# Optimization experiments

Measured on AMD Instinct MI355X. Metric: run time of the kernel, lower is better.

Reference implementation:

```python
import jax, jax.numpy as jnp
import numpy as np

MAX_RADIUS = 10.0
NUM_BASIS = 3
H = 100
C = 32  # dim(Rs_hidden) with scalar-only irreps
LEAKY_SLOPE = 0.01

def swish(v):
    return v * jax.nn.sigmoid(v)


def setup_inputs() -> dict:
    key = jax.random.key(0)
    ks = jax.random.split(key, 10)
    B, N = 4, 256
    x = jax.random.normal(ks[0], (B, N, C), dtype=jnp.float32)
    xyz = jax.random.normal(ks[1], (B, N, 3), dtype=jnp.float32) * 3.0
    mask = jax.random.randint(ks[2], (B, N), 0, 2).astype(jnp.int64)
    # radial MLP (GaussianRadialModel): basis(3) -> h(100) -> C*C path weights
    rw1 = jax.random.normal(ks[3], (NUM_BASIS, H), dtype=jnp.float32) / np.sqrt(NUM_BASIS)
    rw2 = jax.random.normal(ks[4], (H, C * C), dtype=jnp.float32) / np.sqrt(H)
    # fc3: Linear(C, C); fc2: Linear(C, 1)
    fc3_w = jax.random.normal(ks[5], (C, C), dtype=jnp.float32) / np.sqrt(C)
    fc3_b = jax.random.normal(ks[6], (C,), dtype=jnp.float32) * 0.01
    fc2_w = jax.random.normal(ks[7], (C, 1), dtype=jnp.float32) / np.sqrt(C)
    fc2_b = jax.random.normal(ks[8], (1,), dtype=jnp.float32) * 0.01
    return {"x": x, "xyz": xyz, "mask": mask, "rw1": rw1, "rw2": rw2,
            "fc3_w": fc3_w, "fc3_b": fc3_b, "fc2_w": fc2_w, "fc2_b": fc2_b}


def _normalize(v, eps=1e-6):
    mean = jnp.mean(v, axis=-1, keepdims=True)
    std = jnp.std(v, axis=-1, keepdims=True, ddof=1)  # torch std is unbiased
    return (v - mean) / (std + eps)


def reference(x, xyz, mask, rw1, rw2, fc3_w, fc3_b, fc2_w, fc2_b):
    B, N, Cc = x.shape
    # --- fc1: e3nn point convolution with Gaussian radial kernel (l=0 paths) ---
    diff = xyz[:, :, None, :] - xyz[:, None, :, :]            # [B,N,N,3]
    r = jnp.sqrt(jnp.sum(diff * diff, axis=-1) + 1e-12)       # [B,N,N]
    spacing = MAX_RADIUS / NUM_BASIS
    centers = jnp.linspace(0.0, MAX_RADIUS, NUM_BASIS, dtype=jnp.float32)
    gamma = 1.0 / spacing
    basis = jnp.exp(-gamma * (r[..., None] - centers) ** 2)   # [B,N,N,3]
    hid = swish(jnp.einsum('zabk,kh->zabh', basis, rw1))      # [B,N,N,H]
    K = jnp.einsum('zabh,hf->zabf', hid, rw2).reshape(B, N, N, Cc, Cc)  # per-pair kernel
    out = jnp.einsum('zabij,zbj->zai', K, x) / jnp.sqrt(jnp.float32(N))  # [B,N,C]
    # --- Norm(Rs_hidden): per-irrep L2 norm; for l=0 channels this is |x| ---
    out = jnp.abs(out)
    # --- mask + sum pool over points ---
    out = jnp.where(mask[..., None] == 0, 0.0, out)
    pooled = jnp.sum(out, axis=1)                             # [B,C]
    pooled = _normalize(pooled)
    # --- MLP head: leaky_relu(fc3) -> fc2 -> flatten ---
    h1 = pooled @ fc3_w + fc3_b
    h1 = jnp.where(h1 >= 0, h1, LEAKY_SLOPE * h1)
    y = h1 @ fc2_w + fc2_b                                    # [B,1]
    return y.reshape(-1)
```

## Files before the change

### kernel.cpp

```cpp
#include <hip/hip_runtime.h>
#include <math.h>

#define GAMMA 0.3f
#define WSTR3 424

typedef __bf16 bf16x8 __attribute__((ext_vector_type(8)));
typedef __bf16 bf16x4 __attribute__((ext_vector_type(4)));
typedef float  f32x4  __attribute__((ext_vector_type(4)));

__global__ __launch_bounds__(256, 4) void k2_fused(const float* __restrict__ x,
                                                   const float* __restrict__ xyz,
                                                   const float* __restrict__ rw1,
                                                   const float* __restrict__ rw2,
                                                   float* __restrict__ part) {
    __shared__ __bf16 Wlds[32 * WSTR3];
    __shared__ float  rw1s[304];

    int bid = blockIdx.x;
    int ah = bid & 3;
    int hh = (bid >> 2) & 3;
    int bc = (bid >> 4) & 15;
    int z  = bid >> 8;
    int t  = threadIdx.x;
    int w  = t >> 6;
    int l  = t & 63;
    int l16 = l & 15, lg = l >> 4;

    for (int e = t; e < 300; e += 256) rw1s[e] = rw1[e];
    if (t < 128) {
        int icol = t >> 2, g = t & 3;
        *(bf16x4*)&Wlds[icol * WSTR3 + 12 * 32 + g * 8 + 4] = (bf16x4){(__bf16)0.f, (__bf16)0.f, (__bf16)0.f, (__bf16)0.f};
    }

    int a_glob = ah * 64 + w * 16 + l16;
    float ax = xyz[(z * 256 + a_glob) * 3 + 0];
    float ay = xyz[(z * 256 + a_glob) * 3 + 1];
    float az = xyz[(z * 256 + a_glob) * 3 + 2];
    float bas[4][3];
    #pragma unroll
    for (int e = 0; e < 4; ++e) {
        int b_glob = bc * 16 + lg * 4 + e;
        float dx = xyz[(z * 256 + b_glob) * 3 + 0] - ax;
        float dy = xyz[(z * 256 + b_glob) * 3 + 1] - ay;
        float dz = xyz[(z * 256 + b_glob) * 3 + 2] - az;
        float r  = sqrtf(dx * dx + dy * dy + dz * dz + 1e-12f);
        float r5 = r - 5.f, r10 = r - 10.f;
        bas[e][0] = __expf(-GAMMA * r * r);
        bas[e][1] = __expf(-GAMMA * r5 * r5);
        bas[e][2] = __expf(-GAMMA * r10 * r10);
    }

    bf16x8 xa;
    {
        int row = (z * 256 + bc * 16 + l16) * 32;
        float4 v0 = *(const float4*)(x + row + lg * 4);
        float4 v1 = *(const float4*)(x + row + lg * 4 + 16);
        xa[0] = (__bf16)v0.x; xa[1] = (__bf16)v0.y; xa[2] = (__bf16)v0.z; xa[3] = (__bf16)v0.w;
        xa[4] = (__bf16)v1.x; xa[5] = (__bf16)v1.y; xa[6] = (__bf16)v1.z; xa[7] = (__bf16)v1.w;
    }
    for (int q = 0; q < 13; ++q) {
        int nt = q * 4 + w;
        if (nt < 50) {
            int h_loc = nt >> 1;
            int h = hh * 25 + h_loc;
            int ks = h_loc >> 1, hpar = h_loc & 1;
            int icol = ((nt & 1) << 4) + l16;
            const float* rp = rw2 + h * 1024 + icol * 32 + lg * 4;
            float4 r0 = *(const float4*)rp;
            float4 r1 = *(const float4*)(rp + 16);
            bf16x8 rb;
            rb[0] = (__bf16)r0.x; rb[1] = (__bf16)r0.y; rb[2] = (__bf16)r0.z; rb[3] = (__bf16)r0.w;
            rb[4] = (__bf16)r1.x; rb[5] = (__bf16)r1.y; rb[6] = (__bf16)r1.z; rb[7] = (__bf16)r1.w;
            f32x4 d = {0.f, 0.f, 0.f, 0.f};
            d = __builtin_amdgcn_mfma_f32_16x16x32_bf16(xa, rb, d, 0, 0, 0);
            bf16x4 pk;
            pk[0] = (__bf16)d[0]; pk[1] = (__bf16)d[1]; pk[2] = (__bf16)d[2]; pk[3] = (__bf16)d[3];
            *(bf16x4*)&Wlds[icol * WSTR3 + ks * 32 + lg * 8 + hpar * 4] = pk;
        }
    }
    __syncthreads();

    f32x4 acc0 = {0.f, 0.f, 0.f, 0.f};
    f32x4 acc1 = {0.f, 0.f, 0.f, 0.f};
    for (int ks = 0; ks < 12; ++ks) {
        int h0 = hh * 25 + 2 * ks;
        float u00 = rw1s[h0],       u01 = rw1s[h0 + 1];
        float u10 = rw1s[100 + h0], u11 = rw1s[101 + h0];
        float u20 = rw1s[200 + h0], u21 = rw1s[201 + h0];
        bf16x8 af;
        #pragma unroll
        for (int e = 0; e < 4; ++e) {
            float p0 = bas[e][0] * u00 + bas[e][1] * u10 + bas[e][2] * u20;
            float p1 = bas[e][0] * u01 + bas[e][1] * u11 + bas[e][2] * u21;
            float s0 = p0 * __builtin_amdgcn_rcpf(1.f + __expf(-p0));
            float s1 = p1 * __builtin_amdgcn_rcpf(1.f + __expf(-p1));
            af[e]     = (__bf16)s0;
            af[e + 4] = (__bf16)s1;
        }
        int kb = ks * 32 + lg * 8;
        bf16x8 bf0 = *(const bf16x8*)&Wlds[l16 * WSTR3 + kb];
        bf16x8 bf1 = *(const bf16x8*)&Wlds[(16 + l16) * WSTR3 + kb];
        acc0 = __builtin_amdgcn_mfma_f32_16x16x32_bf16(af, bf0, acc0, 0, 0, 0);
        acc1 = __builtin_amdgcn_mfma_f32_16x16x32_bf16(af, bf1, acc1, 0, 0, 0);
    }
    {
        int h0 = hh * 25 + 24;
        float u00 = rw1s[h0], u10 = rw1s[100 + h0], u20 = rw1s[200 + h0];
        bf16x8 af;
        #pragma unroll
        for (int e = 0; e < 4; ++e) {
            float p0 = bas[e][0] * u00 + bas[e][1] * u10 + bas[e][2] * u20;
            float s0 = p0 * __builtin_amdgcn_rcpf(1.f + __expf(-p0));
            af[e]     = (__bf16)s0;
            af[e + 4] = (__bf16)0.f;
        }
        int kb = 12 * 32 + lg * 8;
        bf16x8 bf0 = *(const bf16x8*)&Wlds[l16 * WSTR3 + kb];
        bf16x8 bf1 = *(const bf16x8*)&Wlds[(16 + l16) * WSTR3 + kb];
        acc0 = __builtin_amdgcn_mfma_f32_16x16x32_bf16(af, bf0, acc0, 0, 0, 0);
        acc1 = __builtin_amdgcn_mfma_f32_16x16x32_bf16(af, bf1, acc1, 0, 0, 0);
    }

    int qc = bc * 4 + hh;
    #pragma unroll
    for (int r = 0; r < 4; ++r) {
        int a = ah * 64 + w * 16 + lg * 4 + r;
        size_t base = ((size_t)(z * 64 + qc) * 256 + a) * 32;
        part[base + l16]      = acc0[r];
        part[base + 16 + l16] = acc1[r];
    }
}

__global__ __launch_bounds__(256) void k3a_reduce(const float* __restrict__ part,
                                                  const int* __restrict__ mask,
                                                  float* __restrict__ pooled_part) {
    int blk = blockIdx.x;
    int z = blk >> 6, ag = blk & 63;
    int t = threadIdx.x;
    int i = t & 31;
    int qg = (t >> 5) & 1;
    int a_loc = t >> 6;
    int a = ag * 4 + a_loc;
    const float* base = part + ((size_t)z * 64 * 256 + (size_t)a) * 32 + i;
    float s = 0.f;
    for (int q = qg; q < 64; q += 2)
        s += base[(size_t)q * 8192];
    __shared__ float buf[4][2][32];
    buf[a_loc][qg][i] = s;
    __syncthreads();
    if (t < 128) {
        int al = t >> 5, ii = t & 31;
        float v = buf[al][0][ii] + buf[al][1][ii];
        float sc = (mask[z * 256 + ag * 4 + al] != 0) ? 0.0625f : 0.f;
        buf[al][0][ii] = fabsf(v) * sc;
    }
    __syncthreads();
    if (t < 32) {
        float v = buf[0][0][t] + buf[1][0][t] + buf[2][0][t] + buf[3][0][t];
        pooled_part[(z * 64 + ag) * 32 + t] = v;
    }
}

__global__ __launch_bounds__(128) void k3b_final(const float* __restrict__ pooled_part,
                                                 const float* __restrict__ fc3_w,
                                                 const float* __restrict__ fc3_b,
                                                 const float* __restrict__ fc2_w,
                                                 const float* __restrict__ fc2_b,
                                                 float* __restrict__ out) {
    int t = threadIdx.x;
    int z = t >> 5, i = t & 31;
    float s = 0.f;
    for (int ag = 0; ag < 64; ++ag) s += pooled_part[(z * 64 + ag) * 32 + i];
    float sm = s;
    #pragma unroll
    for (int off = 16; off; off >>= 1) sm += __shfl_xor(sm, off, 32);
    float mean = sm * (1.f / 32.f);
    float d = s - mean;
    float ss = d * d;
    #pragma unroll
    for (int off = 16; off; off >>= 1) ss += __shfl_xor(ss, off, 32);
    float stdv = sqrtf(ss * (1.f / 31.f));
    float nv = d / (stdv + 1e-6f);
    __shared__ float pn[4][32];
    pn[z][i] = nv;
    __syncthreads();
    float h1 = fc3_b[i];
    #pragma unroll
    for (int j = 0; j < 32; ++j) h1 += pn[z][j] * fc3_w[j * 32 + i];
    h1 = (h1 >= 0.f) ? h1 : 0.01f * h1;
    float y = h1 * fc2_w[i];
    #pragma unroll
    for (int off = 16; off; off >>= 1) y += __shfl_xor(y, off, 32);
    if (i == 0) out[z] = y + fc2_b[0];
}

extern "C" void kernel_launch(void* const* d_in, const int* in_sizes, int n_in,
                              void* d_out, int out_size, void* d_ws, size_t ws_size,
                              hipStream_t stream) {
    const float* x    = (const float*)d_in[0];
    const float* xyz  = (const float*)d_in[1];
    const int*   mask = (const int*)d_in[2];
    const float* rw1  = (const float*)d_in[3];
    const float* rw2  = (const float*)d_in[4];
    const float* fc3w = (const float*)d_in[5];
    const float* fc3b = (const float*)d_in[6];
    const float* fc2w = (const float*)d_in[7];
    const float* fc2b = (const float*)d_in[8];
    float* out = (float*)d_out;

    float* part        = (float*)d_ws;
    float* pooled_part = (float*)((char*)d_ws + 8388608);

    hipLaunchKernelGGL(k2_fused,   dim3(1024), dim3(256), 0, stream, x, xyz, rw1, rw2, part);
    hipLaunchKernelGGL(k3a_reduce, dim3(256),  dim3(256), 0, stream, part, mask, pooled_part);
    hipLaunchKernelGGL(k3b_final,  dim3(1),    dim3(128), 0, stream, pooled_part, fc3w, fc3b, fc2w, fc2b, out);
}
```

Baseline: 41.60 us.

## Split per-block W=x·rw2 precompute into separate kernel and stage via global

Moves the x·rw2 MFMA product, previously recomputed inside each fused block (redundantly across the four ah blocks), into a new kernel that writes bf16 W tiles to workspace in a layout matching the LDS consumption order. The main kernel then loads its 25 KB tile with coalesced uint4 loads issued before the basis computation, so the latency overlaps that work. The LDS layout and B-fragment reads change to use two bf16x4 loads per fragment. This adds a kernel launch and a global round trip of about 6.5 MB. It also adds unroll pragmas to the reduction loops.

```diff
diff --git a/kernel.cpp b/kernel.cpp
--- a/kernel.cpp
+++ b/kernel.cpp
@@ -2,18 +2,52 @@
 #include <math.h>
 
 #define GAMMA 0.3f
-#define WSTR3 424
 
 typedef __bf16 bf16x8 __attribute__((ext_vector_type(8)));
 typedef __bf16 bf16x4 __attribute__((ext_vector_type(4)));
 typedef float  f32x4  __attribute__((ext_vector_type(4)));
 
-__global__ __launch_bounds__(256, 4) void k2_fused(const float* __restrict__ x,
-                                                   const float* __restrict__ xyz,
-                                                   const float* __restrict__ rw1,
-                                                   const float* __restrict__ rw2,
-                                                   float* __restrict__ part) {
-    __shared__ __bf16 Wlds[32 * WSTR3];
+__global__ __launch_bounds__(256) void k1_W(const float* __restrict__ x,
+                                            const float* __restrict__ rw2,
+                                            __bf16* __restrict__ Wg) {
+    int bid = blockIdx.x;
+    int mt = bid / 25, nq = bid % 25;
+    int z = mt >> 4, bc = mt & 15;
+    int t = threadIdx.x, w = t >> 6, l = t & 63;
+    int l16 = l & 15, lg = l >> 4;
+
+    int row = (z * 256 + bc * 16 + l16) * 32;
+    float4 v0 = *(const float4*)(x + row + lg * 4);
+    float4 v1 = *(const float4*)(x + row + lg * 4 + 16);
+    bf16x8 xa;
+    xa[0] = (__bf16)v0.x; xa[1] = (__bf16)v0.y; xa[2] = (__bf16)v0.z; xa[3] = (__bf16)v0.w;
+    xa[4] = (__bf16)v1.x; xa[5] = (__bf16)v1.y; xa[6] = (__bf16)v1.z; xa[7] = (__bf16)v1.w;
+
+    #pragma unroll
+    for (int q = 0; q < 2; ++q) {
+        int nt = nq * 8 + w * 2 + q;
+        int h = nt >> 1;
+        int icol = ((nt & 1) << 4) + l16;
+        const float* rp = rw2 + h * 1024 + icol * 32 + lg * 4;
+        float4 r0 = *(const float4*)rp;
+        float4 r1 = *(const float4*)(rp + 16);
+        bf16x8 rb;
+        rb[0] = (__bf16)r0.x; rb[1] = (__bf16)r0.y; rb[2] = (__bf16)r0.z; rb[3] = (__bf16)r0.w;
+        rb[4] = (__bf16)r1.x; rb[5] = (__bf16)r1.y; rb[6] = (__bf16)r1.z; rb[7] = (__bf16)r1.w;
+        f32x4 d = {0.f, 0.f, 0.f, 0.f};
+        d = __builtin_amdgcn_mfma_f32_16x16x32_bf16(xa, rb, d, 0, 0, 0);
+        bf16x4 pk;
+        pk[0] = (__bf16)d[0]; pk[1] = (__bf16)d[1]; pk[2] = (__bf16)d[2]; pk[3] = (__bf16)d[3];
+        size_t off = (((size_t)(z * 16 + bc) * 100 + h) * 32 + icol) * 16 + lg * 4;
+        *(bf16x4*)(Wg + off) = pk;
+    }
+}
+
+__global__ __launch_bounds__(256, 4) void k2_main(const __bf16* __restrict__ Wg,
+                                                  const float* __restrict__ xyz,
+                                                  const float* __restrict__ rw1,
+                                                  float* __restrict__ part) {
+    __shared__ __bf16 Wlds[12800];
     __shared__ float  rw1s[304];
 
     int bid = blockIdx.x;
@@ -27,10 +61,12 @@
     int l16 = l & 15, lg = l >> 4;
 
     for (int e = t; e < 300; e += 256) rw1s[e] = rw1[e];
-    if (t < 128) {
-        int icol = t >> 2, g = t & 3;
-        *(bf16x4*)&Wlds[icol * WSTR3 + 12 * 32 + g * 8 + 4] = (bf16x4){(__bf16)0.f, (__bf16)0.f, (__bf16)0.f, (__bf16)0.f};
-    }
+
+    const uint4* gs = (const uint4*)(Wg + ((size_t)(z * 16 + bc) * 51200 + (size_t)hh * 12800));
+    uint4 stg[7];
+    #pragma unroll
+    for (int j = 0; j < 6; ++j) stg[j] = gs[t + j * 256];
+    if (t < 64) stg[6] = gs[t + 1536];
 
     int a_glob = ah * 64 + w * 16 + l16;
     float ax = xyz[(z * 256 + a_glob) * 3 + 0];
@@ -50,43 +86,18 @@
         bas[e][2] = __expf(-GAMMA * r10 * r10);
     }
 
-    bf16x8 xa;
-    {
-        int row = (z * 256 + bc * 16 + l16) * 32;
-        float4 v0 = *(const float4*)(x + row + lg * 4);
-        float4 v1 = *(const float4*)(x + row + lg * 4 + 16);
-        xa[0] = (__bf16)v0.x; xa[1] = (__bf16)v0.y; xa[2] = (__bf16)v0.z; xa[3] = (__bf16)v0.w;
-        xa[4] = (__bf16)v1.x; xa[5] = (__bf16)v1.y; xa[6] = (__bf16)v1.z; xa[7] = (__bf16)v1.w;
-    }
-    for (int q = 0; q < 13; ++q) {
-        int nt = q * 4 + w;
-        if (nt < 50) {
-            int h_loc = nt >> 1;
-            int h = hh * 25 + h_loc;
-            int ks = h_loc >> 1, hpar = h_loc & 1;
-            int icol = ((nt & 1) << 4) + l16;
-            const float* rp = rw2 + h * 1024 + icol * 32 + lg * 4;
-            float4 r0 = *(const float4*)rp;
-            float4 r1 = *(const float4*)(rp + 16);
-            bf16x8 rb;
-            rb[0] = (__bf16)r0.x; rb[1] = (__bf16)r0.y; rb[2] = (__bf16)r0.z; rb[3] = (__bf16)r0.w;
-            rb[4] = (__bf16)r1.x; rb[5] = (__bf16)r1.y; rb[6] = (__bf16)r1.z; rb[7] = (__bf16)r1.w;
-            f32x4 d = {0.f, 0.f, 0.f, 0.f};
-            d = __builtin_amdgcn_mfma_f32_16x16x32_bf16(xa, rb, d, 0, 0, 0);
-            bf16x4 pk;
-            pk[0] = (__bf16)d[0]; pk[1] = (__bf16)d[1]; pk[2] = (__bf16)d[2]; pk[3] = (__bf16)d[3];
-            *(bf16x4*)&Wlds[icol * WSTR3 + ks * 32 + lg * 8 + hpar * 4] = pk;
-        }
-    }
+    #pragma unroll
+    for (int j = 0; j < 6; ++j) ((uint4*)Wlds)[t + j * 256] = stg[j];
+    if (t < 64) ((uint4*)Wlds)[t + 1536] = stg[6];
     __syncthreads();
 
     f32x4 acc0 = {0.f, 0.f, 0.f, 0.f};
     f32x4 acc1 = {0.f, 0.f, 0.f, 0.f};
     for (int ks = 0; ks < 12; ++ks) {
-        int h0 = hh * 25 + 2 * ks;
-        float u00 = rw1s[h0],       u01 = rw1s[h0 + 1];
-        float u10 = rw1s[100 + h0], u11 = rw1s[101 + h0];
-        float u20 = rw1s[200 + h0], u21 = rw1s[201 + h0];
+        int h0g = hh * 25 + 2 * ks;
+        float u00 = rw1s[h0g],       u01 = rw1s[h0g + 1];
+        float u10 = rw1s[100 + h0g], u11 = rw1s[101 + h0g];
+        float u20 = rw1s[200 + h0g], u21 = rw1s[201 + h0g];
         bf16x8 af;
         #pragma unroll
         for (int e = 0; e < 4; ++e) {
@@ -97,15 +108,19 @@
             af[e]     = (__bf16)s0;
             af[e + 4] = (__bf16)s1;
         }
-        int kb = ks * 32 + lg * 8;
-        bf16x8 bf0 = *(const bf16x8*)&Wlds[l16 * WSTR3 + kb];
-        bf16x8 bf1 = *(const bf16x8*)&Wlds[(16 + l16) * WSTR3 + kb];
+        int b0 = (2 * ks) * 512 + l16 * 16 + lg * 4;
+        bf16x4 a0 = *(const bf16x4*)&Wlds[b0];
+        bf16x4 a1 = *(const bf16x4*)&Wlds[b0 + 512];
+        bf16x4 c0 = *(const bf16x4*)&Wlds[b0 + 256];
+        bf16x4 c1 = *(const bf16x4*)&Wlds[b0 + 512 + 256];
+        bf16x8 bf0 = __builtin_shufflevector(a0, a1, 0, 1, 2, 3, 4, 5, 6, 7);
+        bf16x8 bf1 = __builtin_shufflevector(c0, c1, 0, 1, 2, 3, 4, 5, 6, 7);
         acc0 = __builtin_amdgcn_mfma_f32_16x16x32_bf16(af, bf0, acc0, 0, 0, 0);
         acc1 = __builtin_amdgcn_mfma_f32_16x16x32_bf16(af, bf1, acc1, 0, 0, 0);
     }
     {
-        int h0 = hh * 25 + 24;
-        float u00 = rw1s[h0], u10 = rw1s[100 + h0], u20 = rw1s[200 + h0];
+        int h0g = hh * 25 + 24;
+        float u00 = rw1s[h0g], u10 = rw1s[100 + h0g], u20 = rw1s[200 + h0g];
         bf16x8 af;
         #pragma unroll
         for (int e = 0; e < 4; ++e) {
@@ -114,9 +129,12 @@
             af[e]     = (__bf16)s0;
             af[e + 4] = (__bf16)0.f;
         }
-        int kb = 12 * 32 + lg * 8;
-        bf16x8 bf0 = *(const bf16x8*)&Wlds[l16 * WSTR3 + kb];
-        bf16x8 bf1 = *(const bf16x8*)&Wlds[(16 + l16) * WSTR3 + kb];
+        bf16x4 zz = {(__bf16)0.f, (__bf16)0.f, (__bf16)0.f, (__bf16)0.f};
+        int b0 = 24 * 512 + l16 * 16 + lg * 4;
+        bf16x4 a0 = *(const bf16x4*)&Wlds[b0];
+        bf16x4 c0 = *(const bf16x4*)&Wlds[b0 + 256];
+        bf16x8 bf0 = __builtin_shufflevector(a0, zz, 0, 1, 2, 3, 4, 5, 6, 7);
+        bf16x8 bf1 = __builtin_shufflevector(c0, zz, 0, 1, 2, 3, 4, 5, 6, 7);
         acc0 = __builtin_amdgcn_mfma_f32_16x16x32_bf16(af, bf0, acc0, 0, 0, 0);
         acc1 = __builtin_amdgcn_mfma_f32_16x16x32_bf16(af, bf1, acc1, 0, 0, 0);
     }
@@ -143,6 +161,7 @@
     int a = ag * 4 + a_loc;
     const float* base = part + ((size_t)z * 64 * 256 + (size_t)a) * 32 + i;
     float s = 0.f;
+    #pragma unroll 8
     for (int q = qg; q < 64; q += 2)
         s += base[(size_t)q * 8192];
     __shared__ float buf[4][2][32];
@@ -170,6 +189,7 @@
     int t = threadIdx.x;
     int z = t >> 5, i = t & 31;
     float s = 0.f;
+    #pragma unroll 8
     for (int ag = 0; ag < 64; ++ag) s += pooled_part[(z * 64 + ag) * 32 + i];
     float sm = s;
     #pragma unroll
@@ -208,10 +228,12 @@
     const float* fc2b = (const float*)d_in[8];
     float* out = (float*)d_out;
 
-    float* part        = (float*)d_ws;
-    float* pooled_part = (float*)((char*)d_ws + 8388608);
-
-    hipLaunchKernelGGL(k2_fused,   dim3(1024), dim3(256), 0, stream, x, xyz, rw1, rw2, part);
+    __bf16* Wg         = (__bf16*)d_ws;
+    float*  part       = (float*)((char*)d_ws + 6553600);
+    float*  pooled_part= (float*)((char*)d_ws + 6553600 + 8388608);
+
+    hipLaunchKernelGGL(k1_W,       dim3(1600), dim3(256), 0, stream, x, rw2, Wg);
+    hipLaunchKernelGGL(k2_main,    dim3(1024), dim3(256), 0, stream, Wg, xyz, rw1, part);
     hipLaunchKernelGGL(k3a_reduce, dim3(256),  dim3(256), 0, stream, part, mask, pooled_part);
     hipLaunchKernelGGL(k3b_final,  dim3(1),    dim3(128), 0, stream, pooled_part, fc3w, fc3b, fc2w, fc2b, out);
 }
```

Measured after the change: 43.66 us. 5.0% more time.
